# Performance work log

Hardware: AMD Instinct MI355X
Metric: run time of the kernel (lower is better)

The kernel has to match this reference:

```python
import jax, jax.numpy as jnp
import numpy as np

D_MODEL = 1024
NUM_HEADS = 16
D_K = D_MODEL // NUM_HEADS
ROPE_THETA = 10000.0


def setup_inputs() -> dict:
    key = jax.random.key(0)
    kx, kq, kk, kv, ko = jax.random.split(key, 5)
    B, S = 2, 2048
    sigma = np.sqrt(2.0) / np.sqrt(D_MODEL + D_MODEL)
    x = jax.random.normal(kx, (B, S, D_MODEL), dtype=jnp.float32)
    Wq = jax.random.normal(kq, (D_MODEL, D_MODEL), dtype=jnp.float32) * sigma
    Wk = jax.random.normal(kk, (D_MODEL, D_MODEL), dtype=jnp.float32) * sigma
    Wv = jax.random.normal(kv, (D_MODEL, D_MODEL), dtype=jnp.float32) * sigma
    Wo = jax.random.normal(ko, (D_MODEL, D_MODEL), dtype=jnp.float32) * sigma
    return {"x": x, "Wq": Wq, "Wk": Wk, "Wv": Wv, "Wo": Wo}


def _rope(t, positions):
    # t: [B, H, S, D_K], positions: [S]
    half = jnp.arange(0, D_K, 2, dtype=jnp.float32)          # [D_K/2]
    freqs = 1.0 / (ROPE_THETA ** (half / D_K))               # [D_K/2]
    angles = positions[:, None].astype(jnp.float32) * freqs  # [S, D_K/2]
    cos = jnp.cos(angles)
    sin = jnp.sin(angles)
    t_even = t[..., 0::2]
    t_odd = t[..., 1::2]
    even_rot = t_even * cos - t_odd * sin
    odd_rot = t_even * sin + t_odd * cos
    # interleave back to [..., D_K]
    return jnp.stack([even_rot, odd_rot], axis=-1).reshape(t.shape)


def reference(x, Wq, Wk, Wv, Wo):
    B, S, _ = x.shape
    # weight layout is [d_out, d_in]: y = x @ W.T
    def proj(W):
        y = jnp.einsum('bsd,ed->bse', x, W)
        return y.reshape(B, S, NUM_HEADS, D_K).transpose(0, 2, 1, 3)  # [B,H,S,Dk]
    Q, K, V = proj(Wq), proj(Wk), proj(Wv)
    positions = jnp.arange(S)
    Q = _rope(Q, positions)
    K = _rope(K, positions)
    scale = 1.0 / jnp.sqrt(jnp.asarray(D_K, dtype=x.dtype))
    scores = jnp.einsum('bhqd,bhkd->bhqk', Q, K) * scale  # [B,H,S,S]
    causal = jnp.tril(jnp.ones((S, S), dtype=bool))
    scores = jnp.where(causal, scores, -jnp.inf)
    probs = jax.nn.softmax(scores, axis=-1)
    out = jnp.einsum('bhqk,bhkd->bhqd', probs, V)          # [B,H,S,Dk]
    out = out.transpose(0, 2, 1, 3).reshape(B, S, D_MODEL)
    return jnp.einsum('bsd,ed->bse', out, Wo)
```

## Files before the change

### kernel.cpp

```cpp
#include <hip/hip_runtime.h>
#include <hip/hip_bf16.h>
#include <math.h>

#define S_LEN   2048
#define BATCH   2
#define DMODEL  1024
#define NHEADS  16
#define DKH     64
#define MROWS   (BATCH * S_LEN)

typedef __attribute__((ext_vector_type(8))) __bf16 bf16x8;
typedef __attribute__((ext_vector_type(4))) float f32x4;
typedef __attribute__((ext_vector_type(8))) unsigned short u16x8;

__device__ __forceinline__ float bfu2f(unsigned short u) {
    union { unsigned int i; float f; } v;
    v.i = ((unsigned int)u) << 16;
    return v.f;
}

__device__ __forceinline__ unsigned short f2bfu(float f) {
    union { __bf16 h; unsigned short u; } v;
    v.h = (__bf16)f;
    return v.u;
}

#define LGKM0() __builtin_amdgcn_s_waitcnt(0xc07f)

__device__ __forceinline__ void gload_lds16(const void* g, void* l) {
    __builtin_amdgcn_global_load_lds(
        (const __attribute__((address_space(1))) void*)g,
        (__attribute__((address_space(3))) void*)l, 16, 0, 0);
}

__global__ __launch_bounds__(256) void cvt_all(
    const float* __restrict__ W0, const float* __restrict__ W1, const float* __restrict__ W2,
    const float* __restrict__ X,
    unsigned short* __restrict__ Wb,
    unsigned short* __restrict__ Xb)
{
    const int y = blockIdx.y;
    const float* src;
    unsigned short* dst;
    if (y < 3) {
        src = (y == 0) ? W0 : (y == 1) ? W1 : W2;
        dst = Wb + (size_t)y * (DMODEL * DMODEL);
    } else {
        src = X + (size_t)(y - 3) * (DMODEL * DMODEL);
        dst = Xb + (size_t)(y - 3) * (DMODEL * DMODEL);
    }
    size_t idx = ((size_t)blockIdx.x * 256 + threadIdx.x) * 8;
    float4 a = *(const float4*)(src + idx);
    float4 b = *(const float4*)(src + idx + 4);
    u16x8 h;
    h[0] = f2bfu(a.x); h[1] = f2bfu(a.y); h[2] = f2bfu(a.z); h[3] = f2bfu(a.w);
    h[4] = f2bfu(b.x); h[5] = f2bfu(b.y); h[6] = f2bfu(b.z); h[7] = f2bfu(b.w);
    *(u16x8*)(dst + idx) = h;
}

__global__ __launch_bounds__(256) void cvt_wo(
    const float* __restrict__ W, unsigned short* __restrict__ Wob)
{
    size_t idx = ((size_t)blockIdx.x * 256 + threadIdx.x) * 8;
    float4 a = *(const float4*)(W + idx);
    float4 b = *(const float4*)(W + idx + 4);
    u16x8 h;
    h[0] = f2bfu(a.x); h[1] = f2bfu(a.y); h[2] = f2bfu(a.z); h[3] = f2bfu(a.w);
    h[4] = f2bfu(b.x); h[5] = f2bfu(b.y); h[6] = f2bfu(b.z); h[7] = f2bfu(b.w);
    *(u16x8*)(Wob + idx) = h;
}

__global__ __launch_bounds__(256) void gemm_qkv(
    const unsigned short* __restrict__ Xb,
    const unsigned short* __restrict__ Wb,
    unsigned short* __restrict__ Yq, unsigned short* __restrict__ Yk, unsigned short* __restrict__ Yv)
{
    __shared__ __align__(16) unsigned char pool[36864];
    unsigned short* base = (unsigned short*)pool;

    const int tid  = threadIdx.x;
    const int wave = tid >> 6;
    const int lane = tid & 63;
    const int c    = lane & 15;
    const int quad = lane >> 4;

    const int m0 = blockIdx.y * 128;
    const int n0 = blockIdx.x * 128;
    const int w_idx = n0 >> 10;
    const int e0    = n0 & 1023;
    const unsigned short* Wsrc = Wb + (size_t)w_idx * (DMODEL * DMODEL);

    const int mhalf = (wave & 1) * 64;
    const int nhalf = (wave >> 1) * 64;

    f32x4 acc[4][4];
#pragma unroll
    for (int i = 0; i < 4; i++)
#pragma unroll
        for (int j = 0; j < 4; j++) acc[i][j] = (f32x4){0.f, 0.f, 0.f, 0.f};

    const int srow = wave * 32 + (lane >> 2);
    const int scol = (lane & 3) * 8;
    const unsigned short* Asrc = Xb   + (size_t)(m0 + srow) * DMODEL + scol;
    const unsigned short* Bsrc = Wsrc + (size_t)(e0 + srow) * DMODEL + scol;
    const int doff = srow * 32 + scol;

#define QKV_STAGE(buf, k0) do {                                                    \
    unsigned short* _A = base + (buf) * 8192;                                      \
    unsigned short* _B = _A + 4096;                                                \
    _Pragma("unroll")                                                              \
    for (int _j = 0; _j < 2; _j++) {                                               \
        gload_lds16(Asrc + (size_t)(_j * 16) * DMODEL + (k0), _A + doff + _j * 512);\
        gload_lds16(Bsrc + (size_t)(_j * 16) * DMODEL + (k0), _B + doff + _j * 512);\
    }                                                                              \
} while (0)

#define QKV_COMPUTE(buf) do {                                                      \
    const unsigned short* _A = base + (buf) * 8192;                                \
    const unsigned short* _B = _A + 4096;                                          \
    bf16x8 af[4], bfr[4];                                                          \
    _Pragma("unroll")                                                              \
    for (int mt = 0; mt < 4; mt++)                                                 \
        af[mt] = *(const bf16x8*)(&_A[(mhalf + mt * 16 + c) * 32 + quad * 8]);     \
    _Pragma("unroll")                                                              \
    for (int nt = 0; nt < 4; nt++)                                                 \
        bfr[nt] = *(const bf16x8*)(&_B[(nhalf + nt * 16 + c) * 32 + quad * 8]);    \
    _Pragma("unroll")                                                              \
    for (int mt = 0; mt < 4; mt++)                                                 \
        _Pragma("unroll")                                                          \
        for (int nt = 0; nt < 4; nt++)                                             \
            acc[mt][nt] = __builtin_amdgcn_mfma_f32_16x16x32_bf16(af[mt], bfr[nt], acc[mt][nt], 0, 0, 0); \
} while (0)

    QKV_STAGE(0, 0);
    __syncthreads();
    for (int k0 = 0; k0 < DMODEL - 64; k0 += 64) {
        QKV_STAGE(1, k0 + 32);
        QKV_COMPUTE(0);
        __syncthreads();
        QKV_STAGE(0, k0 + 64);
        QKV_COMPUTE(1);
        __syncthreads();
    }
    QKV_STAGE(1, DMODEL - 32);
    QKV_COMPUTE(0);
    __syncthreads();
    QKV_COMPUTE(1);

    __syncthreads();

    const int h = (e0 + nhalf) >> 6;
    if (w_idx < 2) {
        unsigned short* Yqk = (w_idx == 0) ? Yq : Yk;
        float* EPf = (float*)pool + wave * 16 * 68;
        const int row = lane >> 2;
        const int cg  = lane & 3;
#pragma unroll
        for (int mt = 0; mt < 4; mt++) {
            LGKM0();
#pragma unroll
            for (int nt = 0; nt < 4; nt++)
#pragma unroll
                for (int r = 0; r < 4; r++)
                    EPf[(quad * 4 + r) * 68 + nt * 16 + c] = acc[mt][nt][r];
            LGKM0();
            float fl[16];
#pragma unroll
            for (int j = 0; j < 4; j++) {
                float4 v = *(const float4*)(&EPf[row * 68 + cg * 16 + j * 4]);
                fl[j * 4 + 0] = v.x; fl[j * 4 + 1] = v.y;
                fl[j * 4 + 2] = v.z; fl[j * 4 + 3] = v.w;
            }
            int m = m0 + mhalf + mt * 16 + row;
            int s = m & (S_LEN - 1);
            int b = m >> 11;
            u16x8 o0, o1;
#pragma unroll
            for (int pi = 0; pi < 8; pi++) {
                int p = cg * 8 + pi;
                float freq  = exp2f(-(float)p * 0.41524101186092034f);
                float angle = (float)s * freq;
                float sn, cs;
                __sincosf(angle, &sn, &cs);
                float ev = fl[2 * pi], ov = fl[2 * pi + 1];
                float re = ev * cs - ov * sn;
                float ro = ev * sn + ov * cs;
                if (pi < 4) { o0[2 * pi] = f2bfu(re); o0[2 * pi + 1] = f2bfu(ro); }
                else        { o1[2 * (pi - 4)] = f2bfu(re); o1[2 * (pi - 4) + 1] = f2bfu(ro); }
            }
            unsigned short* dst = Yqk + (((size_t)(b * NHEADS + h)) * S_LEN + s) * DKH + cg * 16;
            *(u16x8*)(dst)     = o0;
            *(u16x8*)(dst + 8) = o1;
        }
    } else {
        unsigned short* EPb = (unsigned short*)pool + wave * 64 * 72;
        LGKM0();
#pragma unroll
        for (int nt = 0; nt < 4; nt++)
#pragma unroll
            for (int mt = 0; mt < 4; mt++)
#pragma unroll
                for (int r = 0; r < 4; r++)
                    EPb[(nt * 16 + c) * 72 + mt * 16 + quad * 4 + r] = f2bfu(acc[mt][nt][r]);
        LGKM0();
        int mbase = m0 + mhalf;
        int s0 = mbase & (S_LEN - 1);
        int b  = mbase >> 11;
        unsigned short* dst = Yv + (((size_t)(b * NHEADS + h)) * DKH + lane) * S_LEN + s0;
#pragma unroll
        for (int j = 0; j < 8; j++)
            *(u16x8*)(dst + j * 8) = *(const u16x8*)(&EPb[lane * 72 + j * 8]);
    }
#undef QKV_STAGE
#undef QKV_COMPUTE
}

__global__ __launch_bounds__(256) void gemm_wo(
    const unsigned short* __restrict__ X,
    const unsigned short* __restrict__ Wob,
    float* __restrict__ Yf)
{
    __shared__ __align__(16) unsigned char pool[24576];
    unsigned short* base = (unsigned short*)pool;

    const int tid  = threadIdx.x;
    const int wave = tid >> 6;
    const int lane = tid & 63;
    const int c    = lane & 15;
    const int quad = lane >> 4;

    const int m0 = blockIdx.y * 64;
    const int n0 = blockIdx.x * 128;

    const int mhalf = (wave & 1) * 32;
    const int nhalf = (wave >> 1) * 64;

    f32x4 acc[2][4];
#pragma unroll
    for (int i = 0; i < 2; i++)
#pragma unroll
        for (int j = 0; j < 4; j++) acc[i][j] = (f32x4){0.f, 0.f, 0.f, 0.f};

    const int arow = wave * 16 + (lane >> 2);
    const int brow = wave * 32 + (lane >> 2);
    const int scol = (lane & 3) * 8;
    const unsigned short* Asrc = X   + (size_t)(m0 + arow) * DMODEL + scol;
    const unsigned short* Bsrc = Wob + (size_t)(n0 + brow) * DMODEL + scol;
    const int adoff = arow * 32 + scol;
    const int bdoff = brow * 32 + scol;

#define WO_STAGE(buf, k0) do {                                                     \
    unsigned short* _A = base + (buf) * 6144;                                      \
    unsigned short* _B = _A + 2048;                                                \
    gload_lds16(Asrc + (k0), _A + adoff);                                          \
    _Pragma("unroll")                                                              \
    for (int _j = 0; _j < 2; _j++)                                                 \
        gload_lds16(Bsrc + (size_t)(_j * 16) * DMODEL + (k0), _B + bdoff + _j * 512);\
} while (0)

#define WO_COMPUTE(buf) do {                                                       \
    const unsigned short* _A = base + (buf) * 6144;                                \
    const unsigned short* _B = _A + 2048;                                          \
    bf16x8 af[2], bfr[4];                                                          \
    _Pragma("unroll")                                                              \
    for (int mt = 0; mt < 2; mt++)                                                 \
        af[mt] = *(const bf16x8*)(&_A[(mhalf + mt * 16 + c) * 32 + quad * 8]);     \
    _Pragma("unroll")                                                              \
    for (int nt = 0; nt < 4; nt++)                                                 \
        bfr[nt] = *(const bf16x8*)(&_B[(nhalf + nt * 16 + c) * 32 + quad * 8]);    \
    _Pragma("unroll")                                                              \
    for (int mt = 0; mt < 2; mt++)                                                 \
        _Pragma("unroll")                                                          \
        for (int nt = 0; nt < 4; nt++)                                             \
            acc[mt][nt] = __builtin_amdgcn_mfma_f32_16x16x32_bf16(af[mt], bfr[nt], acc[mt][nt], 0, 0, 0); \
} while (0)

    WO_STAGE(0, 0);
    __syncthreads();
    for (int k0 = 0; k0 < DMODEL - 64; k0 += 64) {
        WO_STAGE(1, k0 + 32);
        WO_COMPUTE(0);
        __syncthreads();
        WO_STAGE(0, k0 + 64);
        WO_COMPUTE(1);
        __syncthreads();
    }
    WO_STAGE(1, DMODEL - 32);
    WO_COMPUTE(0);
    __syncthreads();
    WO_COMPUTE(1);

    __syncthreads();

    float* EPf = (float*)pool + wave * 16 * 68;
    const int row = lane >> 2;
    const int cg  = lane & 3;
#pragma unroll
    for (int mt = 0; mt < 2; mt++) {
        LGKM0();
#pragma unroll
        for (int nt = 0; nt < 4; nt++)
#pragma unroll
            for (int r = 0; r < 4; r++)
                EPf[(quad * 4 + r) * 68 + nt * 16 + c] = acc[mt][nt][r];
        LGKM0();
        int m = m0 + mhalf + mt * 16 + row;
        float* dst = Yf + (size_t)m * DMODEL + n0 + nhalf + cg * 16;
#pragma unroll
        for (int j = 0; j < 4; j++)
            *(float4*)(dst + j * 4) = *(const float4*)(&EPf[row * 68 + cg * 16 + j * 4]);
    }
#undef WO_STAGE
#undef WO_COMPUTE
}

__global__ __launch_bounds__(256, 4) void attn_mfma(
    const unsigned short* __restrict__ Q,
    const unsigned short* __restrict__ K,
    const unsigned short* __restrict__ Vt,
    unsigned short* __restrict__ A)
{
    __shared__ unsigned short Ks[32 * 72];
    __shared__ unsigned short Vs[64 * 40];
    __shared__ unsigned short Plds[4][16 * 40];

    const int tid  = threadIdx.x;
    const int wave = tid >> 6;
    const int lane = tid & 63;
    const int c    = lane & 15;
    const int quad = lane >> 4;

    const int bh = blockIdx.x;
    const int b  = bh >> 4;
    const int h  = bh & 15;
    const int qb = (int)(gridDim.y - 1) - (int)blockIdx.y;
    const int q0b = qb * 64;
    const int q0 = q0b + wave * 16;

    const unsigned short* Qb = Q  + (size_t)bh * S_LEN * DKH;
    const unsigned short* Kb = K  + (size_t)bh * S_LEN * DKH;
    const unsigned short* Vb = Vt + (size_t)bh * DKH * S_LEN;

    bf16x8 qf0 = *(const bf16x8*)(Qb + (q0 + c) * DKH + quad * 8);
    bf16x8 qf1 = *(const bf16x8*)(Qb + (q0 + c) * DKH + 32 + quad * 8);

    f32x4 o0 = {0.f,0.f,0.f,0.f}, o1 = o0, o2 = o0, o3 = o0;
    float l[4] = {0.f, 0.f, 0.f, 0.f};

    unsigned short* Pw = &Plds[wave][0];

    const int my_nkb   = (q0 + 16 + 31) >> 5;
    const int nkb_blk  = (q0b + 64 + 31) >> 5;
    const int kb_full  = (q0 >= 31) ? (((q0 - 31) >> 5) + 1) : 0;

    const int krow  = tid >> 3;
    const int kcol8 = (tid & 7) * 8;
    const int vrow  = tid >> 2;
    const int vcol8 = (tid & 3) * 8;

    uint4 gK = *(const uint4*)(Kb + (size_t)krow * DKH + kcol8);
    uint4 gV = *(const uint4*)(Vb + (size_t)vrow * S_LEN + vcol8);

    for (int kb = 0; kb < nkb_blk; kb++) {
        const int k0 = kb * 32;
        __syncthreads();
        *(uint4*)(&Ks[krow * 72 + kcol8]) = gK;
        *(uint4*)(&Vs[vrow * 40 + vcol8]) = gV;
        __syncthreads();
        if (kb + 1 < nkb_blk) {
            gK = *(const uint4*)(Kb + (size_t)(k0 + 32 + krow) * DKH + kcol8);
            gV = *(const uint4*)(Vb + (size_t)vrow * S_LEN + k0 + 32 + vcol8);
        }
        if (kb < my_nkb) {
            bf16x8 k00 = *(const bf16x8*)(&Ks[c * 72 + quad * 8]);
            bf16x8 k01 = *(const bf16x8*)(&Ks[c * 72 + 32 + quad * 8]);
            bf16x8 k10 = *(const bf16x8*)(&Ks[(16 + c) * 72 + quad * 8]);
            bf16x8 k11 = *(const bf16x8*)(&Ks[(16 + c) * 72 + 32 + quad * 8]);
            f32x4 s0 = {0.f,0.f,0.f,0.f}, s1 = {0.f,0.f,0.f,0.f};
            s0 = __builtin_amdgcn_mfma_f32_16x16x32_bf16(qf0, k00, s0, 0, 0, 0);
            s0 = __builtin_amdgcn_mfma_f32_16x16x32_bf16(qf1, k01, s0, 0, 0, 0);
            s1 = __builtin_amdgcn_mfma_f32_16x16x32_bf16(qf0, k10, s1, 0, 0, 0);
            s1 = __builtin_amdgcn_mfma_f32_16x16x32_bf16(qf1, k11, s1, 0, 0, 0);

            if (kb < kb_full) {
#pragma unroll
                for (int r = 0; r < 4; r++) {
                    float e0 = __expf(s0[r] * 0.125f);
                    float e1 = __expf(s1[r] * 0.125f);
                    unsigned short pb0 = f2bfu(e0);
                    unsigned short pb1 = f2bfu(e1);
                    Pw[(quad * 4 + r) * 40 + c]      = pb0;
                    Pw[(quad * 4 + r) * 40 + 16 + c] = pb1;
                    l[r] += bfu2f(pb0) + bfu2f(pb1);
                }
            } else {
#pragma unroll
                for (int r = 0; r < 4; r++) {
                    int qrow = q0 + quad * 4 + r;
                    float e0 = (k0 + c      <= qrow) ? __expf(s0[r] * 0.125f) : 0.0f;
                    float e1 = (k0 + 16 + c <= qrow) ? __expf(s1[r] * 0.125f) : 0.0f;
                    unsigned short pb0 = f2bfu(e0);
                    unsigned short pb1 = f2bfu(e1);
                    Pw[(quad * 4 + r) * 40 + c]      = pb0;
                    Pw[(quad * 4 + r) * 40 + 16 + c] = pb1;
                    l[r] += bfu2f(pb0) + bfu2f(pb1);
                }
            }
            LGKM0();

            bf16x8 pf = *(const bf16x8*)(Pw + c * 40 + quad * 8);

            bf16x8 vf0 = *(const bf16x8*)(&Vs[(0 * 16 + c) * 40 + quad * 8]);
            bf16x8 vf1 = *(const bf16x8*)(&Vs[(1 * 16 + c) * 40 + quad * 8]);
            bf16x8 vf2 = *(const bf16x8*)(&Vs[(2 * 16 + c) * 40 + quad * 8]);
            bf16x8 vf3 = *(const bf16x8*)(&Vs[(3 * 16 + c) * 40 + quad * 8]);
            o0 = __builtin_amdgcn_mfma_f32_16x16x32_bf16(pf, vf0, o0, 0, 0, 0);
            o1 = __builtin_amdgcn_mfma_f32_16x16x32_bf16(pf, vf1, o1, 0, 0, 0);
            o2 = __builtin_amdgcn_mfma_f32_16x16x32_bf16(pf, vf2, o2, 0, 0, 0);
            o3 = __builtin_amdgcn_mfma_f32_16x16x32_bf16(pf, vf3, o3, 0, 0, 0);
        }
    }

#pragma unroll
    for (int m = 1; m < 16; m <<= 1) {
#pragma unroll
        for (int r = 0; r < 4; r++) l[r] += __shfl_xor(l[r], m, 64);
    }

#pragma unroll
    for (int r = 0; r < 4; r++) {
        float inv = 1.0f / l[r];
        int s = q0 + quad * 4 + r;
        unsigned short* Ap = A + ((size_t)b * S_LEN + s) * DMODEL + h * DKH;
        Ap[0 * 16 + c] = f2bfu(o0[r] * inv);
        Ap[1 * 16 + c] = f2bfu(o1[r] * inv);
        Ap[2 * 16 + c] = f2bfu(o2[r] * inv);
        Ap[3 * 16 + c] = f2bfu(o3[r] * inv);
    }
}

extern "C" void kernel_launch(void* const* d_in, const int* in_sizes, int n_in,
                              void* d_out, int out_size, void* d_ws, size_t ws_size,
                              hipStream_t stream) {
    const float* x  = (const float*)d_in[0];
    const float* Wq = (const float*)d_in[1];
    const float* Wk = (const float*)d_in[2];
    const float* Wv = (const float*)d_in[3];
    const float* Wo = (const float*)d_in[4];
    float* out = (float*)d_out;

    unsigned short* Qw = (unsigned short*)d_ws;
    unsigned short* Kw = Qw + (size_t)MROWS * DMODEL;
    unsigned short* Vw = Kw + (size_t)MROWS * DMODEL;
    unsigned short* Wb = Vw + (size_t)MROWS * DMODEL;
    unsigned short* Aw = Wb;
    unsigned short* Wob = Qw;
    unsigned short* Xb = (unsigned short*)d_out;

    cvt_all<<<dim3(DMODEL * DMODEL / (256 * 8), 7), 256, 0, stream>>>(Wq, Wk, Wv, x, Wb, Xb);

    gemm_qkv<<<dim3(3 * DMODEL / 128, MROWS / 128), 256, 0, stream>>>(
        Xb, Wb, Qw, Kw, Vw);

    attn_mfma<<<dim3(NHEADS * BATCH, S_LEN / 64), 256, 0, stream>>>(Qw, Kw, Vw, Aw);

    cvt_wo<<<dim3(DMODEL * DMODEL / (256 * 8)), 256, 0, stream>>>(Wo, Wob);

    gemm_wo<<<dim3(DMODEL / 128, MROWS / 64), 256, 0, stream>>>(Aw, Wob, out);
}
```

Baseline: 195.4 us.

## Triple-buffer GEMM LDS pipelines and double-buffer attention K/V tiles

Both projection GEMMs move from a double-buffered loop with full __syncthreads to a three-stage LDS ring. Each stage waits on a partial vmcnt before the barrier, so two tiles of global-to-LDS loads stay in flight while one is computed. The attention kernel double-buffers its K/V shared tiles, which drops one barrier per iteration and writes the next tile after compute. It also raises wave priority around the MFMA groups. LDS use grows, which may lower occupancy, and the hand-tuned vmcnt counts must match the number of loads issued per stage.

```diff
diff --git a/kernel.cpp b/kernel.cpp
--- a/kernel.cpp
+++ b/kernel.cpp
@@ -26,6 +26,12 @@
 }
 
 #define LGKM0() __builtin_amdgcn_s_waitcnt(0xc07f)
+
+#define VMCNT_BAR(n) do {                                        \
+    asm volatile("s_waitcnt vmcnt(" #n ")" ::: "memory");        \
+    __builtin_amdgcn_s_barrier();                                \
+    __builtin_amdgcn_sched_barrier(0);                           \
+} while (0)
 
 __device__ __forceinline__ void gload_lds16(const void* g, void* l) {
     __builtin_amdgcn_global_load_lds(
@@ -75,7 +81,7 @@
     const unsigned short* __restrict__ Wb,
     unsigned short* __restrict__ Yq, unsigned short* __restrict__ Yk, unsigned short* __restrict__ Yv)
 {
-    __shared__ __align__(16) unsigned char pool[36864];
+    __shared__ __align__(16) unsigned char pool[49152];
     unsigned short* base = (unsigned short*)pool;
 
     const int tid  = threadIdx.x;
@@ -105,13 +111,14 @@
     const unsigned short* Bsrc = Wsrc + (size_t)(e0 + srow) * DMODEL + scol;
     const int doff = srow * 32 + scol;
 
-#define QKV_STAGE(buf, k0) do {                                                    \
+#define QKV_STAGE(buf, kt) do {                                                    \
     unsigned short* _A = base + (buf) * 8192;                                      \
     unsigned short* _B = _A + 4096;                                                \
+    const int _k0 = (kt) * 32;                                                     \
     _Pragma("unroll")                                                              \
     for (int _j = 0; _j < 2; _j++) {                                               \
-        gload_lds16(Asrc + (size_t)(_j * 16) * DMODEL + (k0), _A + doff + _j * 512);\
-        gload_lds16(Bsrc + (size_t)(_j * 16) * DMODEL + (k0), _B + doff + _j * 512);\
+        gload_lds16(Asrc + (size_t)(_j * 16) * DMODEL + _k0, _A + doff + _j * 512);\
+        gload_lds16(Bsrc + (size_t)(_j * 16) * DMODEL + _k0, _B + doff + _j * 512);\
     }                                                                              \
 } while (0)
 
@@ -133,19 +140,15 @@
 } while (0)
 
     QKV_STAGE(0, 0);
-    __syncthreads();
-    for (int k0 = 0; k0 < DMODEL - 64; k0 += 64) {
-        QKV_STAGE(1, k0 + 32);
-        QKV_COMPUTE(0);
-        __syncthreads();
-        QKV_STAGE(0, k0 + 64);
-        QKV_COMPUTE(1);
-        __syncthreads();
-    }
-    QKV_STAGE(1, DMODEL - 32);
-    QKV_COMPUTE(0);
-    __syncthreads();
-    QKV_COMPUTE(1);
+    QKV_STAGE(1, 1);
+    for (int g = 0; g < 10; ++g) {
+        const int t = g * 3;
+        VMCNT_BAR(4); QKV_STAGE(2, t + 2); QKV_COMPUTE(0);
+        VMCNT_BAR(4); QKV_STAGE(0, t + 3); QKV_COMPUTE(1);
+        VMCNT_BAR(4); QKV_STAGE(1, t + 4); QKV_COMPUTE(2);
+    }
+    VMCNT_BAR(4); QKV_COMPUTE(0);
+    VMCNT_BAR(0); QKV_COMPUTE(1);
 
     __syncthreads();
 
@@ -220,7 +223,7 @@
     const unsigned short* __restrict__ Wob,
     float* __restrict__ Yf)
 {
-    __shared__ __align__(16) unsigned char pool[24576];
+    __shared__ __align__(16) unsigned char pool[36864];
     unsigned short* base = (unsigned short*)pool;
 
     const int tid  = threadIdx.x;
@@ -249,13 +252,14 @@
     const int adoff = arow * 32 + scol;
     const int bdoff = brow * 32 + scol;
 
-#define WO_STAGE(buf, k0) do {                                                     \
+#define WO_STAGE(buf, kt) do {                                                     \
     unsigned short* _A = base + (buf) * 6144;                                      \
     unsigned short* _B = _A + 2048;                                                \
-    gload_lds16(Asrc + (k0), _A + adoff);                                          \
+    const int _k0 = (kt) * 32;                                                     \
+    gload_lds16(Asrc + _k0, _A + adoff);                                           \
     _Pragma("unroll")                                                              \
     for (int _j = 0; _j < 2; _j++)                                                 \
-        gload_lds16(Bsrc + (size_t)(_j * 16) * DMODEL + (k0), _B + bdoff + _j * 512);\
+        gload_lds16(Bsrc + (size_t)(_j * 16) * DMODEL + _k0, _B + bdoff + _j * 512);\
 } while (0)
 
 #define WO_COMPUTE(buf) do {                                                       \
@@ -276,19 +280,15 @@
 } while (0)
 
     WO_STAGE(0, 0);
-    __syncthreads();
-    for (int k0 = 0; k0 < DMODEL - 64; k0 += 64) {
-        WO_STAGE(1, k0 + 32);
-        WO_COMPUTE(0);
-        __syncthreads();
-        WO_STAGE(0, k0 + 64);
-        WO_COMPUTE(1);
-        __syncthreads();
-    }
-    WO_STAGE(1, DMODEL - 32);
-    WO_COMPUTE(0);
-    __syncthreads();
-    WO_COMPUTE(1);
+    WO_STAGE(1, 1);
+    for (int g = 0; g < 10; ++g) {
+        const int t = g * 3;
+        VMCNT_BAR(3); WO_STAGE(2, t + 2); WO_COMPUTE(0);
+        VMCNT_BAR(3); WO_STAGE(0, t + 3); WO_COMPUTE(1);
+        VMCNT_BAR(3); WO_STAGE(1, t + 4); WO_COMPUTE(2);
+    }
+    VMCNT_BAR(3); WO_COMPUTE(0);
+    VMCNT_BAR(0); WO_COMPUTE(1);
 
     __syncthreads();
 
@@ -320,8 +320,8 @@
     const unsigned short* __restrict__ Vt,
     unsigned short* __restrict__ A)
 {
-    __shared__ unsigned short Ks[32 * 72];
-    __shared__ unsigned short Vs[64 * 40];
+    __shared__ unsigned short Ks[2][32 * 72];
+    __shared__ unsigned short Vs[2][64 * 40];
     __shared__ unsigned short Plds[4][16 * 40];
 
     const int tid  = threadIdx.x;
@@ -360,27 +360,32 @@
 
     uint4 gK = *(const uint4*)(Kb + (size_t)krow * DKH + kcol8);
     uint4 gV = *(const uint4*)(Vb + (size_t)vrow * S_LEN + vcol8);
+    *(uint4*)(&Ks[0][krow * 72 + kcol8]) = gK;
+    *(uint4*)(&Vs[0][vrow * 40 + vcol8]) = gV;
 
     for (int kb = 0; kb < nkb_blk; kb++) {
         const int k0 = kb * 32;
+        const int nb = kb + 1;
+        const bool pre = nb < nkb_blk;
         __syncthreads();
-        *(uint4*)(&Ks[krow * 72 + kcol8]) = gK;
-        *(uint4*)(&Vs[vrow * 40 + vcol8]) = gV;
-        __syncthreads();
-        if (kb + 1 < nkb_blk) {
-            gK = *(const uint4*)(Kb + (size_t)(k0 + 32 + krow) * DKH + kcol8);
-            gV = *(const uint4*)(Vb + (size_t)vrow * S_LEN + k0 + 32 + vcol8);
+        if (pre) {
+            gK = *(const uint4*)(Kb + (size_t)(nb * 32 + krow) * DKH + kcol8);
+            gV = *(const uint4*)(Vb + (size_t)vrow * S_LEN + nb * 32 + vcol8);
         }
         if (kb < my_nkb) {
-            bf16x8 k00 = *(const bf16x8*)(&Ks[c * 72 + quad * 8]);
-            bf16x8 k01 = *(const bf16x8*)(&Ks[c * 72 + 32 + quad * 8]);
-            bf16x8 k10 = *(const bf16x8*)(&Ks[(16 + c) * 72 + quad * 8]);
-            bf16x8 k11 = *(const bf16x8*)(&Ks[(16 + c) * 72 + 32 + quad * 8]);
+            const unsigned short* Kc = &Ks[kb & 1][0];
+            const unsigned short* Vc = &Vs[kb & 1][0];
+            bf16x8 k00 = *(const bf16x8*)(&Kc[c * 72 + quad * 8]);
+            bf16x8 k01 = *(const bf16x8*)(&Kc[c * 72 + 32 + quad * 8]);
+            bf16x8 k10 = *(const bf16x8*)(&Kc[(16 + c) * 72 + quad * 8]);
+            bf16x8 k11 = *(const bf16x8*)(&Kc[(16 + c) * 72 + 32 + quad * 8]);
             f32x4 s0 = {0.f,0.f,0.f,0.f}, s1 = {0.f,0.f,0.f,0.f};
+            __builtin_amdgcn_s_setprio(1);
             s0 = __builtin_amdgcn_mfma_f32_16x16x32_bf16(qf0, k00, s0, 0, 0, 0);
             s0 = __builtin_amdgcn_mfma_f32_16x16x32_bf16(qf1, k01, s0, 0, 0, 0);
             s1 = __builtin_amdgcn_mfma_f32_16x16x32_bf16(qf0, k10, s1, 0, 0, 0);
             s1 = __builtin_amdgcn_mfma_f32_16x16x32_bf16(qf1, k11, s1, 0, 0, 0);
+            __builtin_amdgcn_s_setprio(0);
 
             if (kb < kb_full) {
 #pragma unroll
@@ -410,14 +415,20 @@
 
             bf16x8 pf = *(const bf16x8*)(Pw + c * 40 + quad * 8);
 
-            bf16x8 vf0 = *(const bf16x8*)(&Vs[(0 * 16 + c) * 40 + quad * 8]);
-            bf16x8 vf1 = *(const bf16x8*)(&Vs[(1 * 16 + c) * 40 + quad * 8]);
-            bf16x8 vf2 = *(const bf16x8*)(&Vs[(2 * 16 + c) * 40 + quad * 8]);
-            bf16x8 vf3 = *(const bf16x8*)(&Vs[(3 * 16 + c) * 40 + quad * 8]);
+            bf16x8 vf0 = *(const bf16x8*)(&Vc[(0 * 16 + c) * 40 + quad * 8]);
+            bf16x8 vf1 = *(const bf16x8*)(&Vc[(1 * 16 + c) * 40 + quad * 8]);
+            bf16x8 vf2 = *(const bf16x8*)(&Vc[(2 * 16 + c) * 40 + quad * 8]);
+            bf16x8 vf3 = *(const bf16x8*)(&Vc[(3 * 16 + c) * 40 + quad * 8]);
+            __builtin_amdgcn_s_setprio(1);
             o0 = __builtin_amdgcn_mfma_f32_16x16x32_bf16(pf, vf0, o0, 0, 0, 0);
             o1 = __builtin_amdgcn_mfma_f32_16x16x32_bf16(pf, vf1, o1, 0, 0, 0);
             o2 = __builtin_amdgcn_mfma_f32_16x16x32_bf16(pf, vf2, o2, 0, 0, 0);
             o3 = __builtin_amdgcn_mfma_f32_16x16x32_bf16(pf, vf3, o3, 0, 0, 0);
+            __builtin_amdgcn_s_setprio(0);
+        }
+        if (pre) {
+            *(uint4*)(&Ks[nb & 1][krow * 72 + kcol8]) = gK;
+            *(uint4*)(&Vs[nb & 1][vrow * 40 + vcol8]) = gV;
         }
     }
 
```

After: 190.7 us. 1.02x faster.
